# Performance work log

Hardware: AMD Instinct MI355X
Metric: run time of the kernel (lower is better)

Reference implementation:

```python
import jax, jax.numpy as jnp
import numpy as np
from jax import lax

N_LEVELS = 16
N_NODES = 65536  # nodes per level (= batch_size of trees at the root level)
FEATURES = 7
HIDDEN = 64


def setup_inputs() -> dict:
    key = jax.random.key(0)
    ks = jax.random.split(key, 11)
    contents = jax.random.normal(ks[0], (N_LEVELS, N_NODES, FEATURES), dtype=jnp.float32)
    children = jax.random.randint(ks[1], (N_LEVELS - 1, N_NODES, 2), 0, N_NODES, dtype=jnp.int32)
    s = 0.05
    return {
        'contents': contents,
        'children': children,
        'Wu': jax.random.normal(ks[2], (HIDDEN, FEATURES), dtype=jnp.float32) * s,
        'bu': jax.random.normal(ks[3], (HIDDEN,), dtype=jnp.float32) * s,
        'Wr': jax.random.normal(ks[4], (3 * HIDDEN, 3 * HIDDEN), dtype=jnp.float32) * s,
        'br': jax.random.normal(ks[5], (3 * HIDDEN,), dtype=jnp.float32) * s,
        'Wh': jax.random.normal(ks[6], (HIDDEN, 3 * HIDDEN), dtype=jnp.float32) * s,
        'bh': jax.random.normal(ks[7], (HIDDEN,), dtype=jnp.float32) * s,
        'Wz': jax.random.normal(ks[8], (4 * HIDDEN, 4 * HIDDEN), dtype=jnp.float32) * s,
        'bz': jax.random.normal(ks[9], (4 * HIDDEN,), dtype=jnp.float32) * s,
    }


def reference(contents, children, Wu, bu, Wr, br, Wh, bh, Wz, bz):
    h = Wu.shape[0]

    def leaf_embed(c):  # fc_u + relu
        return jax.nn.relu(c @ Wu.T + bu)

    # deepest level: all leaves -> up_embedding is just u_k
    up_top = leaf_embed(contents[-1])

    def step(up_next, xs):
        c, ch = xs                      # c: [N,F], ch: [N,2]
        u_k = leaf_embed(c)             # [N,h]
        h_L = up_next[ch[:, 0]]         # gather left children  [N,h]
        h_R = up_next[ch[:, 1]]         # gather right children [N,h]
        hhu = jnp.concatenate([h_L, h_R, u_k], axis=1)          # [N,3h]
        r = jax.nn.sigmoid(hhu @ Wr.T + br)                     # fc_r gate
        h_H = jax.nn.relu((r * hhu) @ Wh.T + bh)                # fc_h
        z = jnp.concatenate([h_H, hhu], axis=-1) @ Wz.T + bz    # [N,4h]
        # torch.stack([z_H,z_L,z_R,z_N],2) -> [N,h,4]; softmax over dim=1 (hidden)
        z = jnp.transpose(z.reshape(-1, 4, h), (0, 2, 1))       # [N,h,4]
        z = jax.nn.softmax(z, axis=1)
        h_new = z[:, :, 0] * h_H + z[:, :, 1] * h_L + z[:, :, 2] * h_R + z[:, :, 3] * u_k
        return h_new, None

    # process levels n-2, ..., 0 (bottom-up)
    xs = (contents[:-1][::-1], children[::-1])
    up0, _ = lax.scan(step, up_top, xs)
    # level 0 has batch_size roots -> h_out shape [batch_size, hidden]
    return up0
```

## Files before the change

### kernel.cpp

```cpp
#include <hip/hip_runtime.h>
#include <math.h>


#define N_NODES 65536
#define FEAT 7
#define H 64
#define MT 16
#define BLK 256

typedef __attribute__((ext_vector_type(8))) short bf16x8;
typedef __attribute__((ext_vector_type(4))) float f32x4;

__device__ __forceinline__ void split_bf16(float x, short& hi, short& lo) {
    unsigned u = __float_as_uint(x);
    unsigned r = (u + 0x7fffu + ((u >> 16) & 1u)) >> 16;
    hi = (short)r;
    float res = x - __uint_as_float(r << 16);
    unsigned u2 = __float_as_uint(res);
    unsigned r2 = (u2 + 0x7fffu + ((u2 >> 16) & 1u)) >> 16;
    lo = (short)r2;
}
__device__ __forceinline__ float bf2f(short h) {
    return __uint_as_float(((unsigned)(unsigned short)h) << 16);
}
__device__ __forceinline__ int zbidx(int row, int col) {
    return row * 192 + ((((col >> 3) ^ (row & 7)) << 3) | (col & 7));
}
__device__ __forceinline__ int zaidx(int row, int col) {
    return row * 64 + ((((col >> 3) ^ (row & 7)) << 3) | (col & 7));
}

#define MFMA3(acc, ah, al, bh8, bl8)                                              \
    acc = __builtin_amdgcn_mfma_f32_16x16x32_bf16(al, bh8, acc, 0, 0, 0);         \
    acc = __builtin_amdgcn_mfma_f32_16x16x32_bf16(ah, bl8, acc, 0, 0, 0);         \
    acc = __builtin_amdgcn_mfma_f32_16x16x32_bf16(ah, bh8, acc, 0, 0, 0);

__global__ __launch_bounds__(256) void grnn_prep(
    const float* __restrict__ Wr, const float* __restrict__ Wh,
    const float* __restrict__ Wz, short* __restrict__ wsp)
{
    int job = blockIdx.x * 4 + (threadIdx.x >> 6);
    int lane = threadIdx.x & 63;
    const float* src; int K, t, s; short* dst;
    short* ws_wh = wsp + 72 * 1024;
    short* ws_wz = wsp + 96 * 1024;
    if (job < 72)       { t = job / 6;            s = job % 6;        K = 192; src = Wr; dst = wsp   + job * 1024; }
    else if (job < 96)  { int j = job - 72; t = j / 6; s = j % 6;     K = 192; src = Wh; dst = ws_wh + j * 1024; }
    else                { int j = job - 96; t = j / 8; s = j % 8;     K = 256; src = Wz; dst = ws_wz + j * 1024; }
    int i  = t * 16 + (lane & 15);
    int k0 = s * 32 + (lane >> 4) * 8;
    const float* p = src + (size_t)i * K + k0;
    bf16x8 hi, lo;
#pragma unroll
    for (int e = 0; e < 8; ++e) { short h, l; split_bf16(p[e], h, l); hi[e] = h; lo[e] = l; }
    *(bf16x8*)(dst + lane * 8) = hi;
    *(bf16x8*)(dst + 512 + lane * 8) = lo;
}

__global__ __launch_bounds__(BLK) void grnn_leaf_bf(
    const float* __restrict__ contents, const float* __restrict__ Wu,
    const float* __restrict__ bu, short* __restrict__ hi_out, short* __restrict__ lo_out)
{
    int t = blockIdx.x * BLK + threadIdx.x;
    int node = t >> 6;
    int j = t & 63;
    const float* c = contents + (size_t)15 * N_NODES * FEAT + (size_t)node * FEAT;
    float acc = bu[j];
#pragma unroll
    for (int f = 0; f < FEAT; ++f) acc += c[f] * Wu[j * FEAT + f];
    short h, l; split_bf16(fmaxf(acc, 0.f), h, l);
    hi_out[t] = h;
    lo_out[t] = l;
}

__global__ __launch_bounds__(BLK) void grnn_leaf_kernel(
    const float* __restrict__ contents, const float* __restrict__ Wu,
    const float* __restrict__ bu, float* __restrict__ h_out)
{
    int t = blockIdx.x * BLK + threadIdx.x;
    int node = t >> 6;
    int j = t & 63;
    const float* c = contents + (size_t)15 * N_NODES * FEAT + (size_t)node * FEAT;
    float acc = bu[j];
#pragma unroll
    for (int f = 0; f < FEAT; ++f) acc += c[f] * Wu[j * FEAT + f];
    h_out[t] = fmaxf(acc, 0.f);
}

__global__ __launch_bounds__(BLK) void grnn_step_mfma(
    const float* __restrict__ contents_k, const int* __restrict__ children_k,
    const short* __restrict__ hin_hi, const short* __restrict__ hin_lo,
    const float* __restrict__ Wu, const float* __restrict__ bu,
    const float* __restrict__ br, const float* __restrict__ bh,
    const float* __restrict__ bz,
    const short* __restrict__ wsp,
    short* __restrict__ hout_hi, short* __restrict__ hout_lo,
    float* __restrict__ out_f32, int is_final)
{
    __shared__ __align__(16) short smem[4 * MT * 192];
    short* zb_hi = smem;
    short* zb_lo = smem + MT * 192;
    short* ub0   = smem + 2 * MT * 192;
    short* ub1   = smem + 3 * MT * 192;
    float* hacc  = (float*)smem;

    const int tid = threadIdx.x;
    const int node0 = blockIdx.x * MT;
    const int wv = tid >> 6, lane = tid & 63, lr = lane & 15, lh = lane >> 4;
    const short* wr_s = wsp;
    const short* wh_s = wsp + 72 * 1024;
    const short* wz_s = wsp + 96 * 1024;
    const f32x4 z4 = {0.f, 0.f, 0.f, 0.f};

    if (tid < 128) {
        int row = tid >> 2, q = tid & 3;
        int nd = row >> 1, side = row & 1;
        int child = children_k[(size_t)(node0 + nd) * 2 + side];
        const bf16x8* srch = (const bf16x8*)(hin_hi + (size_t)child * H + q * 16);
        const bf16x8* srcl = (const bf16x8*)(hin_lo + (size_t)child * H + q * 16);
        int col0 = side * 64 + q * 16;
        int i0 = zbidx(nd, col0);
        int i1 = zbidx(nd, col0 + 8);
        *(bf16x8*)&zb_hi[i0] = srch[0];
        *(bf16x8*)&zb_hi[i1] = srch[1];
        *(bf16x8*)&zb_lo[i0] = srcl[0];
        *(bf16x8*)&zb_lo[i1] = srcl[1];
    } else {
        int t = tid - 128;
        int nd = t >> 3, j0 = (t & 7) * 8;
        float c[FEAT];
#pragma unroll
        for (int f = 0; f < FEAT; ++f) c[f] = contents_k[(size_t)(node0 + nd) * FEAT + f];
        bf16x8 hv, lv;
#pragma unroll
        for (int jj = 0; jj < 8; ++jj) {
            int j = j0 + jj;
            float a = bu[j];
#pragma unroll
            for (int f = 0; f < FEAT; ++f) a += c[f] * Wu[j * FEAT + f];
            a = fmaxf(a, 0.f);
            short h, l; split_bf16(a, h, l); hv[jj] = h; lv[jj] = l;
        }
        int idx = zbidx(nd, 128 + j0);
        *(bf16x8*)&zb_hi[idx] = hv;
        *(bf16x8*)&zb_lo[idx] = lv;
    }
    __syncthreads();

    f32x4 acc1[3] = {z4, z4, z4};
    for (int s = 0; s < 6; ++s) {
        int idx = zbidx(lr, s * 32 + lh * 8);
        bf16x8 ah = *(const bf16x8*)&zb_hi[idx];
        bf16x8 al = *(const bf16x8*)&zb_lo[idx];
#pragma unroll
        for (int ni = 0; ni < 3; ++ni) {
            const short* bp = wr_s + ((3 * wv + ni) * 6 + s) * 1024;
            bf16x8 bh8 = *(const bf16x8*)(bp + lane * 8);
            bf16x8 bl8 = *(const bf16x8*)(bp + 512 + lane * 8);
            MFMA3(acc1[ni], ah, al, bh8, bl8);
        }
    }
#pragma unroll
    for (int ni = 0; ni < 3; ++ni) {
        int i = (3 * wv + ni) * 16 + lr;
        float brv = br[i];
#pragma unroll
        for (int r = 0; r < 4; ++r) {
            int nd = lh * 4 + r;
            float v = acc1[ni][r] + brv;
            float sg = 1.f / (1.f + __expf(-v));
            int xi = zbidx(nd, i);
            float x = bf2f(zb_hi[xi]) + bf2f(zb_lo[xi]);
            short h, l; split_bf16(sg * x, h, l);
            ub0[xi] = h;
            ub1[xi] = l;
        }
    }
    __syncthreads();

    f32x4 acc2 = z4;
    for (int s = 0; s < 6; ++s) {
        int idx = zbidx(lr, s * 32 + lh * 8);
        bf16x8 ah = *(const bf16x8*)&ub0[idx];
        bf16x8 al = *(const bf16x8*)&ub1[idx];
        const short* bp = wh_s + (wv * 6 + s) * 1024;
        bf16x8 bh8 = *(const bf16x8*)(bp + lane * 8);
        bf16x8 bl8 = *(const bf16x8*)(bp + 512 + lane * 8);
        MFMA3(acc2, ah, al, bh8, bl8);
    }
    __syncthreads();
    {
        int j = wv * 16 + lr;
        float bhv = bh[j];
#pragma unroll
        for (int r = 0; r < 4; ++r) {
            int nd = lh * 4 + r;
            float v = fmaxf(acc2[r] + bhv, 0.f);
            short h, l; split_bf16(v, h, l);
            int idx = zaidx(nd, j);
            ub0[idx] = h;
            ub1[idx] = l;
        }
    }
    __syncthreads();

    f32x4 acc3[4] = {z4, z4, z4, z4};
    for (int s = 0; s < 8; ++s) {
        bf16x8 ah, al;
        if (s < 2) {
            int idx = zaidx(lr, s * 32 + lh * 8);
            ah = *(const bf16x8*)&ub0[idx];
            al = *(const bf16x8*)&ub1[idx];
        } else {
            int idx = zbidx(lr, s * 32 + lh * 8 - 64);
            ah = *(const bf16x8*)&zb_hi[idx];
            al = *(const bf16x8*)&zb_lo[idx];
        }
#pragma unroll
        for (int jh = 0; jh < 4; ++jh) {
            const short* bp = wz_s + ((wv * 4 + jh) * 8 + s) * 1024;
            bf16x8 bh8 = *(const bf16x8*)(bp + lane * 8);
            bf16x8 bl8 = *(const bf16x8*)(bp + 512 + lane * 8);
            MFMA3(acc3[jh], ah, al, bh8, bl8);
        }
    }
    float bzv[4];
#pragma unroll
    for (int jh = 0; jh < 4; ++jh) bzv[jh] = bz[wv * 64 + jh * 16 + lr];
    float contrib[4][4];
#pragma unroll
    for (int r = 0; r < 4; ++r) {
        float v0 = acc3[0][r] + bzv[0];
        float v1 = acc3[1][r] + bzv[1];
        float v2 = acc3[2][r] + bzv[2];
        float v3 = acc3[3][r] + bzv[3];
        float mx = fmaxf(fmaxf(v0, v1), fmaxf(v2, v3));
        mx = fmaxf(mx, __shfl_xor(mx, 1));
        mx = fmaxf(mx, __shfl_xor(mx, 2));
        mx = fmaxf(mx, __shfl_xor(mx, 4));
        mx = fmaxf(mx, __shfl_xor(mx, 8));
        float e0 = __expf(v0 - mx), e1 = __expf(v1 - mx);
        float e2 = __expf(v2 - mx), e3 = __expf(v3 - mx);
        float sm = e0 + e1 + e2 + e3;
        sm += __shfl_xor(sm, 1);
        sm += __shfl_xor(sm, 2);
        sm += __shfl_xor(sm, 4);
        sm += __shfl_xor(sm, 8);
        float inv = 1.f / sm;
        int nd = lh * 4 + r;
        float e[4] = {e0, e1, e2, e3};
#pragma unroll
        for (int jh = 0; jh < 4; ++jh) {
            int n = wv * 64 + jh * 16 + lr;
            float comp;
            if (wv == 0) {
                int idx = zaidx(nd, n);
                comp = bf2f(ub0[idx]) + bf2f(ub1[idx]);
            } else {
                int idx = zbidx(nd, n - 64);
                comp = bf2f(zb_hi[idx]) + bf2f(zb_lo[idx]);
            }
            contrib[jh][r] = e[jh] * inv * comp;
        }
    }
    __syncthreads();
    for (int p = 0; p < 4; ++p) {
        if (wv == p) {
#pragma unroll
            for (int r = 0; r < 4; ++r) {
                int nd = lh * 4 + r;
#pragma unroll
                for (int jh = 0; jh < 4; ++jh) {
                    int hidx = nd * 68 + jh * 16 + lr;
                    if (p == 0) hacc[hidx] = contrib[jh][r];
                    else        hacc[hidx] += contrib[jh][r];
                }
            }
        }
        __syncthreads();
    }
    if (is_final) {
#pragma unroll
        for (int it = 0; it < 4; ++it) {
            int i = tid + it * BLK;
            int nd = i >> 6, j = i & 63;
            out_f32[(size_t)(node0 + nd) * H + j] = hacc[nd * 68 + j];
        }
    } else {
#pragma unroll
        for (int it = 0; it < 4; ++it) {
            int i = tid + it * BLK;
            int nd = i >> 6, j = i & 63;
            float v = hacc[nd * 68 + j];
            short h, l; split_bf16(v, h, l);
            size_t o = (size_t)(node0 + nd) * H + j;
            hout_hi[o] = h;
            hout_lo[o] = l;
        }
    }
}

#define HP 196
#define HHP 68
#define ZP 260
#define NT1 16
__global__ __launch_bounds__(BLK) void grnn_step_v1(
    const float* __restrict__ contents_k, const int* __restrict__ children_k,
    const float* __restrict__ h_in,
    const float* __restrict__ Wu, const float* __restrict__ bu,
    const float* __restrict__ Wr, const float* __restrict__ br,
    const float* __restrict__ Wh, const float* __restrict__ bh,
    const float* __restrict__ Wz, const float* __restrict__ bz,
    float* __restrict__ h_out)
{
    __shared__ __align__(16) float hhu[NT1][HP];
    __shared__ __align__(16) float rh[NT1][HP];
    __shared__ __align__(16) float hH[NT1][HHP];
    __shared__ __align__(16) float zt[NT1][ZP];
    __shared__ float rden[NT1][4];
    const int tid = threadIdx.x;
    const int node0 = blockIdx.x * NT1;
    const int n = tid >> 4, c16 = tid & 15;
    {
        const float* cptr = contents_k + (size_t)(node0 + n) * FEAT;
        float cf[FEAT];
#pragma unroll
        for (int f = 0; f < FEAT; ++f) cf[f] = cptr[f];
#pragma unroll
        for (int jj = 0; jj < 4; ++jj) {
            int j = c16 + 16 * jj;
            float acc = bu[j];
#pragma unroll
            for (int f = 0; f < FEAT; ++f) acc += cf[f] * Wu[j * FEAT + f];
            hhu[n][128 + j] = fmaxf(acc, 0.f);
        }
#pragma unroll
        for (int it = 0; it < 8; ++it) {
            int t = tid + it * BLK;
            int nn = t >> 7, side = (t >> 6) & 1, j = t & 63;
            int child = children_k[(size_t)(node0 + nn) * 2 + side];
            hhu[nn][side * 64 + j] = h_in[(size_t)child * H + j];
        }
    }
    __syncthreads();
    {
        float acc[12];
#pragma unroll
        for (int ii = 0; ii < 12; ++ii) acc[ii] = br[c16 + 16 * ii];
        for (int k = 0; k < 192; k += 4) {
            float4 hv = *(const float4*)&hhu[n][k];
#pragma unroll
            for (int ii = 0; ii < 12; ++ii) {
                float4 w = *(const float4*)&Wr[(size_t)(c16 + 16 * ii) * 192 + k];
                acc[ii] += hv.x * w.x + hv.y * w.y + hv.z * w.z + hv.w * w.w;
            }
        }
#pragma unroll
        for (int ii = 0; ii < 12; ++ii) {
            int i = c16 + 16 * ii;
            rh[n][i] = (1.f / (1.f + __expf(-acc[ii]))) * hhu[n][i];
        }
    }
    __syncthreads();
    {
        float acc[4];
#pragma unroll
        for (int ii = 0; ii < 4; ++ii) acc[ii] = bh[c16 + 16 * ii];
        for (int k = 0; k < 192; k += 4) {
            float4 hv = *(const float4*)&rh[n][k];
#pragma unroll
            for (int ii = 0; ii < 4; ++ii) {
                float4 w = *(const float4*)&Wh[(size_t)(c16 + 16 * ii) * 192 + k];
                acc[ii] += hv.x * w.x + hv.y * w.y + hv.z * w.z + hv.w * w.w;
            }
        }
#pragma unroll
        for (int ii = 0; ii < 4; ++ii) hH[n][c16 + 16 * ii] = fmaxf(acc[ii], 0.f);
    }
    __syncthreads();
    {
        float acc[16];
#pragma unroll
        for (int ii = 0; ii < 16; ++ii) acc[ii] = bz[c16 + 16 * ii];
        for (int k = 0; k < 64; k += 4) {
            float4 hv = *(const float4*)&hH[n][k];
#pragma unroll
            for (int ii = 0; ii < 16; ++ii) {
                float4 w = *(const float4*)&Wz[(size_t)(c16 + 16 * ii) * 256 + k];
                acc[ii] += hv.x * w.x + hv.y * w.y + hv.z * w.z + hv.w * w.w;
            }
        }
        for (int k = 0; k < 192; k += 4) {
            float4 hv = *(const float4*)&hhu[n][k];
#pragma unroll
            for (int ii = 0; ii < 16; ++ii) {
                float4 w = *(const float4*)&Wz[(size_t)(c16 + 16 * ii) * 256 + 64 + k];
                acc[ii] += hv.x * w.x + hv.y * w.y + hv.z * w.z + hv.w * w.w;
            }
        }
#pragma unroll
        for (int ii = 0; ii < 16; ++ii) zt[n][c16 + 16 * ii] = acc[ii];
    }
    __syncthreads();
    {
        int sn = tid >> 4, g = (tid >> 2) & 3, q = tid & 3;
        float m = -INFINITY;
#pragma unroll
        for (int jj = 0; jj < 16; ++jj) m = fmaxf(m, zt[sn][g * 64 + q * 16 + jj]);
        m = fmaxf(m, __shfl_xor(m, 1));
        m = fmaxf(m, __shfl_xor(m, 2));
        float s = 0.f;
#pragma unroll
        for (int jj = 0; jj < 16; ++jj) {
            int idx = g * 64 + q * 16 + jj;
            float e = __expf(zt[sn][idx] - m);
            zt[sn][idx] = e;
            s += e;
        }
        s += __shfl_xor(s, 1);
        s += __shfl_xor(s, 2);
        if (q == 0) rden[sn][g] = 1.f / s;
    }
    __syncthreads();
    {
        size_t node = node0 + n;
#pragma unroll
        for (int jj = 0; jj < 4; ++jj) {
            int j = c16 + 16 * jj;
            float v = zt[n][j] * rden[n][0] * hH[n][j]
                    + zt[n][64 + j] * rden[n][1] * hhu[n][j]
                    + zt[n][128 + j] * rden[n][2] * hhu[n][64 + j]
                    + zt[n][192 + j] * rden[n][3] * hhu[n][128 + j];
            h_out[node * H + j] = v;
        }
    }
}

extern "C" void kernel_launch(void* const* d_in, const int* in_sizes, int n_in,
                              void* d_out, int out_size, void* d_ws, size_t ws_size,
                              hipStream_t stream) {
    const float* contents = (const float*)d_in[0];
    const int*   children = (const int*)d_in[1];
    const float* Wu = (const float*)d_in[2];
    const float* bu = (const float*)d_in[3];
    const float* Wr = (const float*)d_in[4];
    const float* br = (const float*)d_in[5];
    const float* Wh = (const float*)d_in[6];
    const float* bh = (const float*)d_in[7];
    const float* Wz = (const float*)d_in[8];
    const float* bz = (const float*)d_in[9];
    float* out = (float*)d_out;
    const size_t HN = (size_t)N_NODES * H;
    const size_t H_BYTES = HN * 4;
    const size_t W_BYTES = (72 + 24 + 128) * 2048;

    if (ws_size >= H_BYTES + W_BYTES) {
        short* A_hi = (short*)d_ws;
        short* A_lo = A_hi + HN;
        short* B_hi = (short*)d_out;
        short* B_lo = B_hi + HN;
        short* wsp  = (short*)((char*)d_ws + H_BYTES);

        grnn_prep<<<56, 256, 0, stream>>>(Wr, Wh, Wz, wsp);
        grnn_leaf_bf<<<(N_NODES * H) / BLK, BLK, 0, stream>>>(contents, Wu, bu, A_hi, A_lo);
        for (int k = 14; k >= 0; --k) {
            const short* in_hi = ((k + 1) & 1) ? A_hi : B_hi;
            const short* in_lo = ((k + 1) & 1) ? A_lo : B_lo;
            short* out_hi = (k & 1) ? A_hi : B_hi;
            short* out_lo = (k & 1) ? A_lo : B_lo;
            grnn_step_mfma<<<N_NODES / MT, BLK, 0, stream>>>(
                contents + (size_t)k * N_NODES * FEAT,
                children + (size_t)k * N_NODES * 2,
                in_hi, in_lo, Wu, bu, br, bh, bz, wsp,
                out_hi, out_lo, out, (k == 0) ? 1 : 0);
        }
    } else {
        float* h_ws = (float*)d_ws;
        grnn_leaf_kernel<<<(N_NODES * H) / BLK, BLK, 0, stream>>>(contents, Wu, bu, h_ws);
        for (int k = 14; k >= 0; --k) {
            const float* hin = (((k + 1) & 1) == 0) ? out : h_ws;
            float* hout = ((k & 1) == 0) ? out : h_ws;
            grnn_step_v1<<<N_NODES / NT1, BLK, 0, stream>>>(
                contents + (size_t)k * N_NODES * FEAT,
                children + (size_t)k * N_NODES * 2,
                hin, Wu, bu, Wr, br, Wh, bh, Wz, bz, hout);
        }
    }
}
```

Measured before the change: 1.333 ms.

## Preload MFMA A-fragments, shorten cross-wave reduction barriers, set min blocks per CU

Each GEMM stage now loads all A-operand fragments from LDS into registers before issuing the MFMA chain, so LDS latency overlaps instead of serialising with each MFMA. The final four-wave serial accumulation, which used four barriers, becomes a two-buffer pairwise reduction with two barriers, and the halves are summed at write-out. Launch bounds also request four blocks per CU. In exchange, the preloaded fragments raise register pressure, and the occupancy hint may force spilling.

Result: no change. 1.330 ms (-0.2%).

```diff
diff --git a/kernel.cpp b/kernel.cpp
--- a/kernel.cpp
+++ b/kernel.cpp
@@ -87,7 +87,7 @@
     h_out[t] = fmaxf(acc, 0.f);
 }
 
-__global__ __launch_bounds__(BLK) void grnn_step_mfma(
+__global__ __launch_bounds__(BLK, 4) void grnn_step_mfma(
     const float* __restrict__ contents_k, const int* __restrict__ children_k,
     const short* __restrict__ hin_hi, const short* __restrict__ hin_lo,
     const float* __restrict__ Wu, const float* __restrict__ bu,
@@ -102,7 +102,8 @@
     short* zb_lo = smem + MT * 192;
     short* ub0   = smem + 2 * MT * 192;
     short* ub1   = smem + 3 * MT * 192;
-    float* hacc  = (float*)smem;
+    float* bufA  = (float*)smem;
+    float* bufB  = (float*)smem + MT * 68;
 
     const int tid = threadIdx.x;
     const int node0 = blockIdx.x * MT;
@@ -148,16 +149,23 @@
     __syncthreads();
 
     f32x4 acc1[3] = {z4, z4, z4};
-    for (int s = 0; s < 6; ++s) {
-        int idx = zbidx(lr, s * 32 + lh * 8);
-        bf16x8 ah = *(const bf16x8*)&zb_hi[idx];
-        bf16x8 al = *(const bf16x8*)&zb_lo[idx];
-#pragma unroll
-        for (int ni = 0; ni < 3; ++ni) {
-            const short* bp = wr_s + ((3 * wv + ni) * 6 + s) * 1024;
-            bf16x8 bh8 = *(const bf16x8*)(bp + lane * 8);
-            bf16x8 bl8 = *(const bf16x8*)(bp + 512 + lane * 8);
-            MFMA3(acc1[ni], ah, al, bh8, bl8);
+    {
+        bf16x8 pah[6], pal[6];
+#pragma unroll
+        for (int s = 0; s < 6; ++s) {
+            int idx = zbidx(lr, s * 32 + lh * 8);
+            pah[s] = *(const bf16x8*)&zb_hi[idx];
+            pal[s] = *(const bf16x8*)&zb_lo[idx];
+        }
+#pragma unroll
+        for (int s = 0; s < 6; ++s) {
+#pragma unroll
+            for (int ni = 0; ni < 3; ++ni) {
+                const short* bp = wr_s + ((3 * wv + ni) * 6 + s) * 1024;
+                bf16x8 bh8 = *(const bf16x8*)(bp + lane * 8);
+                bf16x8 bl8 = *(const bf16x8*)(bp + 512 + lane * 8);
+                MFMA3(acc1[ni], pah[s], pal[s], bh8, bl8);
+            }
         }
     }
 #pragma unroll
@@ -179,14 +187,21 @@
     __syncthreads();
 
     f32x4 acc2 = z4;
-    for (int s = 0; s < 6; ++s) {
-        int idx = zbidx(lr, s * 32 + lh * 8);
-        bf16x8 ah = *(const bf16x8*)&ub0[idx];
-        bf16x8 al = *(const bf16x8*)&ub1[idx];
-        const short* bp = wh_s + (wv * 6 + s) * 1024;
-        bf16x8 bh8 = *(const bf16x8*)(bp + lane * 8);
-        bf16x8 bl8 = *(const bf16x8*)(bp + 512 + lane * 8);
-        MFMA3(acc2, ah, al, bh8, bl8);
+    {
+        bf16x8 pah[6], pal[6];
+#pragma unroll
+        for (int s = 0; s < 6; ++s) {
+            int idx = zbidx(lr, s * 32 + lh * 8);
+            pah[s] = *(const bf16x8*)&ub0[idx];
+            pal[s] = *(const bf16x8*)&ub1[idx];
+        }
+#pragma unroll
+        for (int s = 0; s < 6; ++s) {
+            const short* bp = wh_s + (wv * 6 + s) * 1024;
+            bf16x8 bh8 = *(const bf16x8*)(bp + lane * 8);
+            bf16x8 bl8 = *(const bf16x8*)(bp + 512 + lane * 8);
+            MFMA3(acc2, pah[s], pal[s], bh8, bl8);
+        }
     }
     __syncthreads();
     {
@@ -205,23 +220,48 @@
     __syncthreads();
 
     f32x4 acc3[4] = {z4, z4, z4, z4};
-    for (int s = 0; s < 8; ++s) {
-        bf16x8 ah, al;
-        if (s < 2) {
-            int idx = zaidx(lr, s * 32 + lh * 8);
-            ah = *(const bf16x8*)&ub0[idx];
-            al = *(const bf16x8*)&ub1[idx];
-        } else {
-            int idx = zbidx(lr, s * 32 + lh * 8 - 64);
-            ah = *(const bf16x8*)&zb_hi[idx];
-            al = *(const bf16x8*)&zb_lo[idx];
-        }
-#pragma unroll
-        for (int jh = 0; jh < 4; ++jh) {
-            const short* bp = wz_s + ((wv * 4 + jh) * 8 + s) * 1024;
-            bf16x8 bh8 = *(const bf16x8*)(bp + lane * 8);
-            bf16x8 bl8 = *(const bf16x8*)(bp + 512 + lane * 8);
-            MFMA3(acc3[jh], ah, al, bh8, bl8);
+    {
+        bf16x8 pah[4], pal[4];
+#pragma unroll
+        for (int s = 0; s < 4; ++s) {
+            if (s < 2) {
+                int idx = zaidx(lr, s * 32 + lh * 8);
+                pah[s] = *(const bf16x8*)&ub0[idx];
+                pal[s] = *(const bf16x8*)&ub1[idx];
+            } else {
+                int idx = zbidx(lr, s * 32 + lh * 8 - 64);
+                pah[s] = *(const bf16x8*)&zb_hi[idx];
+                pal[s] = *(const bf16x8*)&zb_lo[idx];
+            }
+        }
+#pragma unroll
+        for (int s = 0; s < 4; ++s) {
+#pragma unroll
+            for (int jh = 0; jh < 4; ++jh) {
+                const short* bp = wz_s + ((wv * 4 + jh) * 8 + s) * 1024;
+                bf16x8 bh8 = *(const bf16x8*)(bp + lane * 8);
+                bf16x8 bl8 = *(const bf16x8*)(bp + 512 + lane * 8);
+                MFMA3(acc3[jh], pah[s], pal[s], bh8, bl8);
+            }
+        }
+    }
+    {
+        bf16x8 pah[4], pal[4];
+#pragma unroll
+        for (int s = 0; s < 4; ++s) {
+            int idx = zbidx(lr, (s + 4) * 32 + lh * 8 - 64);
+            pah[s] = *(const bf16x8*)&zb_hi[idx];
+            pal[s] = *(const bf16x8*)&zb_lo[idx];
+        }
+#pragma unroll
+        for (int s = 0; s < 4; ++s) {
+#pragma unroll
+            for (int jh = 0; jh < 4; ++jh) {
+                const short* bp = wz_s + ((wv * 4 + jh) * 8 + (s + 4)) * 1024;
+                bf16x8 bh8 = *(const bf16x8*)(bp + lane * 8);
+                bf16x8 bl8 = *(const bf16x8*)(bp + 512 + lane * 8);
+                MFMA3(acc3[jh], pah[s], pal[s], bh8, bl8);
+            }
         }
     }
     float bzv[4];
@@ -264,34 +304,41 @@
         }
     }
     __syncthreads();
-    for (int p = 0; p < 4; ++p) {
-        if (wv == p) {
-#pragma unroll
-            for (int r = 0; r < 4; ++r) {
-                int nd = lh * 4 + r;
-#pragma unroll
-                for (int jh = 0; jh < 4; ++jh) {
-                    int hidx = nd * 68 + jh * 16 + lr;
-                    if (p == 0) hacc[hidx] = contrib[jh][r];
-                    else        hacc[hidx] += contrib[jh][r];
-                }
-            }
-        }
-        __syncthreads();
-    }
+    if (wv < 2) {
+        float* buf = (wv == 0) ? bufA : bufB;
+#pragma unroll
+        for (int r = 0; r < 4; ++r) {
+            int nd = lh * 4 + r;
+#pragma unroll
+            for (int jh = 0; jh < 4; ++jh)
+                buf[nd * 68 + jh * 16 + lr] = contrib[jh][r];
+        }
+    }
+    __syncthreads();
+    if (wv >= 2) {
+        float* buf = (wv == 2) ? bufA : bufB;
+#pragma unroll
+        for (int r = 0; r < 4; ++r) {
+            int nd = lh * 4 + r;
+#pragma unroll
+            for (int jh = 0; jh < 4; ++jh)
+                buf[nd * 68 + jh * 16 + lr] += contrib[jh][r];
+        }
+    }
+    __syncthreads();
     if (is_final) {
 #pragma unroll
         for (int it = 0; it < 4; ++it) {
             int i = tid + it * BLK;
             int nd = i >> 6, j = i & 63;
-            out_f32[(size_t)(node0 + nd) * H + j] = hacc[nd * 68 + j];
+            out_f32[(size_t)(node0 + nd) * H + j] = bufA[nd * 68 + j] + bufB[nd * 68 + j];
         }
     } else {
 #pragma unroll
         for (int it = 0; it < 4; ++it) {
             int i = tid + it * BLK;
             int nd = i >> 6, j = i & 63;
-            float v = hacc[nd * 68 + j];
+            float v = bufA[nd * 68 + j] + bufB[nd * 68 + j];
             short h, l; split_bf16(v, h, l);
             size_t o = (size_t)(node0 + nd) * H + j;
             hout_hi[o] = h;
```
